# Performance work log

Measured on AMD Instinct MI355X. Metric: run time of the kernel, lower is better.

The kernel has to match this reference:

```python
import jax, jax.numpy as jnp
import numpy as np

B, N, C, H = 2, 2048, 1024, 16
D = C // H  # head_dim = 64
EPS = 1e-6


def rmsnorm(x, w, eps=EPS):
    # RMSNorm over last dim (head_dim), matching torch RMSNorm (computed in fp32)
    x32 = x.astype(jnp.float32)
    y = x32 * jax.lax.rsqrt(jnp.mean(x32 * x32, axis=-1, keepdims=True) + eps)
    return y.astype(x.dtype) * w


def setup_inputs() -> dict:
    key = jax.random.key(0)
    ks = jax.random.split(key, 4)
    return {
        "x": jax.random.normal(ks[0], (B, N, C), dtype=jnp.float32),
        "w_qkv": jax.random.normal(ks[1], (C, 3 * C), dtype=jnp.float32) * 0.02,
        "b_qkv": jnp.zeros((3 * C,), dtype=jnp.float32),
        "q_w": jnp.ones((D,), dtype=jnp.float32),
        "k_w": jnp.ones((D,), dtype=jnp.float32),
        "w_proj": jax.random.normal(ks[2], (C, C), dtype=jnp.float32) * 0.02,
        "b_proj": jnp.zeros((C,), dtype=jnp.float32),
    }


def reference(x, w_qkv, b_qkv, q_w, k_w, w_proj, b_proj):
    b, n, c = x.shape
    h, d = H, c // H
    # QKV projection -> [3, B, H, N, D]
    qkv = (x @ w_qkv + b_qkv).reshape(b, n, 3, h, d).transpose(2, 0, 3, 1, 4)
    q, k, v = qkv[0], qkv[1], qkv[2]
    # per-head RMSNorm on q/k (qk_norm=True, use_rmsnorm=True)
    q = rmsnorm(q, q_w)
    k = rmsnorm(k, k_w)
    # scaled dot-product attention (scale = head_dim**-0.5, no dropout at eval)
    scale = d ** -0.5
    attn = jax.nn.softmax(jnp.einsum('bhqd,bhkd->bhqk', q, k) * scale, axis=-1)
    out = jnp.einsum('bhqk,bhkd->bhqd', attn, v)  # [B,H,N,D]
    out = out.transpose(0, 2, 1, 3).reshape(b, n, c)
    return out @ w_proj + b_proj
```

## Files before the change

### kernel.cpp

```cpp
#include <hip/hip_runtime.h>

typedef unsigned short u16;
typedef unsigned int u32;
typedef float f4 __attribute__((ext_vector_type(4)));
typedef __bf16 b8 __attribute__((ext_vector_type(8)));
typedef _Float16 h4 __attribute__((ext_vector_type(4)));
typedef __fp16 hp2 __attribute__((ext_vector_type(2)));

#if __has_builtin(__builtin_amdgcn_exp2f)
#define EXP2(x) __builtin_amdgcn_exp2f(x)
#else
#define EXP2(x) exp2f(x)
#endif

__device__ __forceinline__ u16 f2bf(float f) {
  unsigned u = __float_as_uint(f);
  u += 0x7fffu + ((u >> 16) & 1u);
  return (u16)(u >> 16);
}
__device__ __forceinline__ float bf2f(u16 h) {
  return __uint_as_float(((unsigned)h) << 16);
}

__global__ void k_convert_all(const float* __restrict__ x,
                              const float* __restrict__ w_qkv,
                              const float* __restrict__ w_proj,
                              u16* __restrict__ xb, u16* __restrict__ wqkT,
                              u16* __restrict__ wpjT) {
  __shared__ u16 t[64][65];
  int bid = blockIdx.x;
  if (bid < 2048) {
    int i = (bid * 256 + threadIdx.x) * 8;
    float4 a = *(const float4*)(x + i);
    float4 b = *(const float4*)(x + i + 4);
    union { u16 h[8]; uint4 v; } r;
    r.h[0] = f2bf(a.x); r.h[1] = f2bf(a.y); r.h[2] = f2bf(a.z); r.h[3] = f2bf(a.w);
    r.h[4] = f2bf(b.x); r.h[5] = f2bf(b.y); r.h[6] = f2bf(b.z); r.h[7] = f2bf(b.w);
    *(uint4*)(xb + i) = r.v;
    return;
  }
  const float* w; u16* wT; int Ncols, Krows, bx, by;
  if (bid < 2816) { int l = bid - 2048; w = w_qkv; wT = wqkT; Ncols = 3072; Krows = 1024; bx = l % 48; by = l / 48; }
  else            { int l = bid - 2816; w = w_proj; wT = wpjT; Ncols = 1024; Krows = 1024; bx = l & 15; by = l >> 4; }
  int n0 = bx * 64, k0 = by * 64;
#pragma unroll
  for (int it = 0; it < 16; ++it) {
    int e = it * 256 + threadIdx.x;
    int r = e >> 6, c = e & 63;
    t[r][c] = f2bf(w[(size_t)(k0 + r) * Ncols + n0 + c]);
  }
  __syncthreads();
#pragma unroll
  for (int it = 0; it < 4; ++it) {
    int e = it * 256 + threadIdx.x;
    int r = e >> 4, c0 = (e & 15) * 4;
    union { u16 h[4]; uint2 v; } pk;
    pk.h[0] = t[c0][r]; pk.h[1] = t[c0 + 1][r];
    pk.h[2] = t[c0 + 2][r]; pk.h[3] = t[c0 + 3][r];
    *(uint2*)(wT + (size_t)(n0 + r) * Krows + k0 + c0) = pk.v;
  }
}

__global__ __launch_bounds__(256, 3) void k_gemm_qkv(
    const u16* __restrict__ A, const u16* __restrict__ Bt,
    const float* __restrict__ bias,
    u16* __restrict__ oq, u16* __restrict__ ok, u16* __restrict__ ov,
    const float* __restrict__ qw, const float* __restrict__ kw,
    int K) {
  __shared__ u16 lA[2][128 * 32];
  __shared__ u16 lB[2][128 * 32];
  const int tid = threadIdx.x;
  const int lane = tid & 63, lrow = lane & 15, lq = lane >> 4;
  const int wave = tid >> 6;
  const int bm = blockIdx.y * 128, bn = blockIdx.x * 128;
  const int wm = (wave >> 1) * 64, wn = (wave & 1) * 64;

  const int ch0 = tid, ch1 = 256 + tid;
  const u16* ap0 = A + (size_t)(bm + (ch0 >> 2)) * K + (ch0 & 3) * 8;
  const u16* ap1 = A + (size_t)(bm + (ch1 >> 2)) * K + (ch1 & 3) * 8;
  const u16* bp0 = Bt + (size_t)(bn + (ch0 >> 2)) * K + (ch0 & 3) * 8;
  const u16* bp1 = Bt + (size_t)(bn + (ch1 >> 2)) * K + (ch1 & 3) * 8;

  uint4 pA0 = *(const uint4*)ap0, pA1 = *(const uint4*)ap1;
  uint4 pB0 = *(const uint4*)bp0, pB1 = *(const uint4*)bp1;

  f4 acc[4][4] = {};
  const int iters = K >> 5;
  for (int it = 0; it < iters; ++it) {
    const int s = it & 1;
    *(uint4*)(lA[s] + ch0 * 8) = pA0; *(uint4*)(lA[s] + ch1 * 8) = pA1;
    *(uint4*)(lB[s] + ch0 * 8) = pB0; *(uint4*)(lB[s] + ch1 * 8) = pB1;
    if (it + 1 < iters) {
      ap0 += 32; ap1 += 32; bp0 += 32; bp1 += 32;
      pA0 = *(const uint4*)ap0; pA1 = *(const uint4*)ap1;
      pB0 = *(const uint4*)bp0; pB1 = *(const uint4*)bp1;
    }
    __syncthreads();
    b8 af[4], bf[4];
#pragma unroll
    for (int i = 0; i < 4; ++i)
      af[i] = *(const b8*)(lA[s] + (wm + i * 16 + lrow) * 32 + lq * 8);
#pragma unroll
    for (int j = 0; j < 4; ++j)
      bf[j] = *(const b8*)(lB[s] + (wn + j * 16 + lrow) * 32 + lq * 8);
#pragma unroll
    for (int i = 0; i < 4; ++i)
#pragma unroll
      for (int j = 0; j < 4; ++j)
        acc[i][j] = __builtin_amdgcn_mfma_f32_16x16x32_bf16(af[i], bf[j], acc[i][j], 0, 0, 0);
  }

  float bv[4];
#pragma unroll
  for (int j = 0; j < 4; ++j) bv[j] = bias[bn + wn + j * 16 + lrow];

  const float CS = 0.125f * 1.44269504088896340736f;
  const int n0w = bn + wn;
  const int sec = n0w >> 10;
  const int h = (n0w >> 6) & 15;
#pragma unroll
  for (int i = 0; i < 4; ++i) {
    float v[4][4];
#pragma unroll
    for (int j = 0; j < 4; ++j)
#pragma unroll
      for (int r = 0; r < 4; ++r) v[j][r] = acc[i][j][r] + bv[j];
    if (sec < 2) {
      u16* dst = sec == 0 ? oq : ok;
      const float* w = sec == 0 ? qw : kw;
      float ex = sec == 0 ? CS : 1.0f;
#pragma unroll
      for (int r = 0; r < 4; ++r) {
        float ss = v[0][r] * v[0][r] + v[1][r] * v[1][r] +
                   v[2][r] * v[2][r] + v[3][r] * v[3][r];
        ss += __shfl_xor(ss, 1, 64); ss += __shfl_xor(ss, 2, 64);
        ss += __shfl_xor(ss, 4, 64); ss += __shfl_xor(ss, 8, 64);
        float sc = rsqrtf(ss * (1.0f / 64.0f) + 1e-6f) * ex;
        int m = bm + wm + i * 16 + lq * 4 + r;
        int bb = m >> 11, ns = m & 2047;
        u16* rowp = dst + ((size_t)(bb * 16 + h) * 2048 + ns) * 64;
#pragma unroll
        for (int j = 0; j < 4; ++j) {
          int d = j * 16 + lrow;
          rowp[d] = f2bf(v[j][r] * sc * w[d]);
        }
      }
    } else {
      int m0 = bm + wm + i * 16 + lq * 4;
      int bb = m0 >> 11, ns = m0 & 2047;
#pragma unroll
      for (int j = 0; j < 4; ++j) {
        int d = j * 16 + lrow;
        union { _Float16 hh[4]; uint2 u; } pk;
#pragma unroll
        for (int r = 0; r < 4; ++r) pk.hh[r] = (_Float16)v[j][r];
        *(uint2*)(ov + ((size_t)(bb * 16 + h) * 64 + d) * 2048 + ns) = pk.u;
      }
    }
  }
}

__global__ __launch_bounds__(256, 4) void k_gemm2(
    const u16* __restrict__ A, const u16* __restrict__ Bt,
    const float* __restrict__ bias, float* __restrict__ outF,
    int K, int Ncols) {
  __shared__ u16 lA[2][64 * 32];
  __shared__ u16 lB[2][128 * 32];
  const int tid = threadIdx.x;
  const int lane = tid & 63, lrow = lane & 15, lq = lane >> 4;
  const int wave = tid >> 6;
  const int bm = blockIdx.y * 64, bn = blockIdx.x * 128;
  const int wm = (wave >> 1) * 32, wn = (wave & 1) * 64;

  const int cha = tid;
  const int ch0 = tid, ch1 = 256 + tid;
  const u16* ap = A + (size_t)(bm + (cha >> 2)) * K + (cha & 3) * 8;
  const u16* bp0 = Bt + (size_t)(bn + (ch0 >> 2)) * K + (ch0 & 3) * 8;
  const u16* bp1 = Bt + (size_t)(bn + (ch1 >> 2)) * K + (ch1 & 3) * 8;

  uint4 pA = *(const uint4*)ap;
  uint4 pB0 = *(const uint4*)bp0, pB1 = *(const uint4*)bp1;

  f4 acc[2][4] = {};
  const int iters = K >> 5;
  for (int it = 0; it < iters; ++it) {
    const int s = it & 1;
    *(uint4*)(lA[s] + cha * 8) = pA;
    *(uint4*)(lB[s] + ch0 * 8) = pB0; *(uint4*)(lB[s] + ch1 * 8) = pB1;
    if (it + 1 < iters) {
      ap += 32; bp0 += 32; bp1 += 32;
      pA = *(const uint4*)ap;
      pB0 = *(const uint4*)bp0; pB1 = *(const uint4*)bp1;
    }
    __syncthreads();
    b8 af[2], bf[4];
#pragma unroll
    for (int i = 0; i < 2; ++i)
      af[i] = *(const b8*)(lA[s] + (wm + i * 16 + lrow) * 32 + lq * 8);
#pragma unroll
    for (int j = 0; j < 4; ++j)
      bf[j] = *(const b8*)(lB[s] + (wn + j * 16 + lrow) * 32 + lq * 8);
#pragma unroll
    for (int i = 0; i < 2; ++i)
#pragma unroll
      for (int j = 0; j < 4; ++j)
        acc[i][j] = __builtin_amdgcn_mfma_f32_16x16x32_bf16(af[i], bf[j], acc[i][j], 0, 0, 0);
  }
#pragma unroll
  for (int i = 0; i < 2; ++i)
#pragma unroll
    for (int j = 0; j < 4; ++j) {
      int n = bn + wn + j * 16 + lrow;
      float bv = bias[n];
#pragma unroll
      for (int r = 0; r < 4; ++r) {
        int m = bm + wm + i * 16 + lq * 4 + r;
        outF[(size_t)m * Ncols + n] = acc[i][j][r] + bv;
      }
    }
}

__global__ __launch_bounds__(512, 8) void k_attn(
    const u16* __restrict__ qb, const u16* __restrict__ kb,
    const u16* __restrict__ vt, u16* __restrict__ ao) {
  __shared__ u16 lK[128 * 72];
  __shared__ u16 lV[64 * 140];
  const int bh = blockIdx.y;
  const int q0 = blockIdx.x * 64;
  const int tid = threadIdx.x, wave = tid >> 6, lane = tid & 63;
  const int lrow = lane & 15, lq = lane >> 4;
  const int qg = wave & 3;
  const int kh = wave >> 2;
  const int wq = qg * 16;

  b8 qf[2];
#pragma unroll
  for (int ks = 0; ks < 2; ++ks)
    qf[ks] = *(const b8*)(qb + ((size_t)bh * 2048 + q0 + wq + lrow) * 64 + ks * 32 + lq * 8);

  f4 o[4] = {};
  f4 lacc = {};
  h4 ones;
  ones[0] = (_Float16)1.0f; ones[1] = (_Float16)1.0f;
  ones[2] = (_Float16)1.0f; ones[3] = (_Float16)1.0f;

  const int ch0 = tid, ch1 = 512 + tid;
  const u16* kp0 = kb + (size_t)bh * 2048 * 64 + (size_t)(ch0 >> 3) * 64 + (ch0 & 7) * 8;
  const u16* kp1 = kb + (size_t)bh * 2048 * 64 + (size_t)(ch1 >> 3) * 64 + (ch1 & 7) * 8;
  const u16* vp0 = vt + (size_t)bh * 64 * 2048 + (size_t)(ch0 >> 4) * 2048 + (ch0 & 15) * 8;
  const u16* vp1 = vt + (size_t)bh * 64 * 2048 + (size_t)(ch1 >> 4) * 2048 + (ch1 & 15) * 8;
  u16* lKw0 = lK + (ch0 >> 3) * 72 + (ch0 & 7) * 8;
  u16* lKw1 = lK + (ch1 >> 3) * 72 + (ch1 & 7) * 8;
  u16* lVw0 = lV + (ch0 >> 4) * 140 + (ch0 & 15) * 8;
  u16* lVw1 = lV + (ch1 >> 4) * 140 + (ch1 & 15) * 8;

  uint4 pK0 = *(const uint4*)kp0, pK1 = *(const uint4*)kp1;
  uint4 pV0 = *(const uint4*)vp0, pV1 = *(const uint4*)vp1;

  for (int it = 0; it < 16; ++it) {
    *(uint4*)lKw0 = pK0;
    *(uint4*)lKw1 = pK1;
    *(uint2*)lVw0 = make_uint2(pV0.x, pV0.y);
    *(uint2*)(lVw0 + 4) = make_uint2(pV0.z, pV0.w);
    *(uint2*)lVw1 = make_uint2(pV1.x, pV1.y);
    *(uint2*)(lVw1 + 4) = make_uint2(pV1.z, pV1.w);
    __syncthreads();

    if (it < 15) {
      kp0 += 128 * 64; kp1 += 128 * 64; vp0 += 128; vp1 += 128;
      pK0 = *(const uint4*)kp0; pK1 = *(const uint4*)kp1;
      pV0 = *(const uint4*)vp0; pV1 = *(const uint4*)vp1;
    }

    f4 st[4] = {};
#pragma unroll
    for (int ks = 0; ks < 2; ++ks)
#pragma unroll
      for (int kt = 0; kt < 4; ++kt) {
        b8 kf = *(const b8*)(lK + ((kh * 64 + kt * 16) + lrow) * 72 + ks * 32 + lq * 8);
        st[kt] = __builtin_amdgcn_mfma_f32_16x16x32_bf16(kf, qf[ks], st[kt], 0, 0, 0);
      }
#pragma unroll
    for (int kt = 0; kt < 4; ++kt) {
      union { hp2 p2[2]; h4 v; } cv;
      cv.p2[0] = __builtin_amdgcn_cvt_pkrtz(EXP2(st[kt][0]), EXP2(st[kt][1]));
      cv.p2[1] = __builtin_amdgcn_cvt_pkrtz(EXP2(st[kt][2]), EXP2(st[kt][3]));
      h4 pf = cv.v;
      lacc = __builtin_amdgcn_mfma_f32_16x16x16f16(ones, pf, lacc, 0, 0, 0);
#pragma unroll
      for (int dt = 0; dt < 4; ++dt) {
        h4 va = *(const h4*)(lV + (dt * 16 + lrow) * 140 + kh * 64 + kt * 16 + lq * 4);
        o[dt] = __builtin_amdgcn_mfma_f32_16x16x16f16(va, pf, o[dt], 0, 0, 0);
      }
    }
    __syncthreads();
  }

  float* ms = (float*)lK;
  const int base = (qg * 64 + lane) * 17;
  if (kh) {
#pragma unroll
    for (int dt = 0; dt < 4; ++dt)
#pragma unroll
      for (int rr = 0; rr < 4; ++rr) ms[base + dt * 4 + rr] = o[dt][rr];
    ms[base + 16] = lacc[0];
  }
  __syncthreads();
  if (!kh) {
    float inv = 1.0f / (lacc[0] + ms[base + 16]);
    const int bb = bh >> 4, h = bh & 15;
    int q = q0 + wq + lrow;
#pragma unroll
    for (int dt = 0; dt < 4; ++dt) {
      union { u16 h2[4]; uint2 v; } r;
#pragma unroll
      for (int rr = 0; rr < 4; ++rr)
        r.h2[rr] = f2bf((o[dt][rr] + ms[base + dt * 4 + rr]) * inv);
      *(uint2*)(ao + ((size_t)bb * 2048 + q) * 1024 + h * 64 + dt * 16 + lq * 4) = r.v;
    }
  }
}

extern "C" void kernel_launch(void* const* d_in, const int* in_sizes, int n_in,
                              void* d_out, int out_size, void* d_ws, size_t ws_size,
                              hipStream_t stream) {
  const float* x      = (const float*)d_in[0];
  const float* w_qkv  = (const float*)d_in[1];
  const float* b_qkv  = (const float*)d_in[2];
  const float* q_w    = (const float*)d_in[3];
  const float* k_w    = (const float*)d_in[4];
  const float* w_proj = (const float*)d_in[5];
  const float* b_proj = (const float*)d_in[6];
  float* out = (float*)d_out;

  u16* xb   = (u16*)d_ws;
  u16* wqkT = xb + 4194304;
  u16* wpjT = wqkT + 3145728;
  u16* qb   = wpjT + 1048576;
  u16* kb   = qb + 4194304;
  u16* vtb  = kb + 4194304;
  u16* ao   = xb;

  k_convert_all<<<3072, 256, 0, stream>>>(x, w_qkv, w_proj, xb, wqkT, wpjT);
  k_gemm_qkv<<<dim3(24, 32), 256, 0, stream>>>(xb, wqkT, b_qkv, qb, kb, vtb, q_w, k_w, 1024);
  k_attn<<<dim3(32, 32), 512, 0, stream>>>(qb, kb, vtb, ao);
  k_gemm2<<<dim3(8, 64), 256, 0, stream>>>(ao, wpjT, b_proj, out, 1024, 1024);
}
```

Baseline: 195.3 us.

## Enlarge attention query tile to 256 rows and drop key-split reduction

Each attention block now processes 256 queries instead of 64, with each wave owning 32 query rows over the full 128-key tile rather than splitting keys across two wave halves. This reuses each K/V tile loaded into LDS across four times as many queries and removes the cross-wave LDS merge of partial outputs and sums at the end. In exchange the grid drops to 256 blocks, about one per CU on this device, and register pressure roughly doubles per wave, which may reduce occupancy and latency hiding.

```diff
diff --git a/kernel.cpp b/kernel.cpp
--- a/kernel.cpp
+++ b/kernel.cpp
@@ -220,26 +220,27 @@
     }
 }
 
-__global__ __launch_bounds__(512, 8) void k_attn(
+__global__ __launch_bounds__(512, 2) void k_attn(
     const u16* __restrict__ qb, const u16* __restrict__ kb,
     const u16* __restrict__ vt, u16* __restrict__ ao) {
   __shared__ u16 lK[128 * 72];
   __shared__ u16 lV[64 * 140];
   const int bh = blockIdx.y;
-  const int q0 = blockIdx.x * 64;
+  const int q0 = blockIdx.x * 256;
   const int tid = threadIdx.x, wave = tid >> 6, lane = tid & 63;
   const int lrow = lane & 15, lq = lane >> 4;
-  const int qg = wave & 3;
-  const int kh = wave >> 2;
-  const int wq = qg * 16;
-
-  b8 qf[2];
-#pragma unroll
-  for (int ks = 0; ks < 2; ++ks)
-    qf[ks] = *(const b8*)(qb + ((size_t)bh * 2048 + q0 + wq + lrow) * 64 + ks * 32 + lq * 8);
-
-  f4 o[4] = {};
-  f4 lacc = {};
+  const int wq = wave * 32;
+
+  b8 qf[2][2];
+#pragma unroll
+  for (int g = 0; g < 2; ++g)
+#pragma unroll
+    for (int ks = 0; ks < 2; ++ks)
+      qf[g][ks] = *(const b8*)(qb + ((size_t)bh * 2048 + q0 + wq + g * 16 + lrow) * 64 +
+                               ks * 32 + lq * 8);
+
+  f4 o[2][4] = {};
+  f4 lacc[2] = {};
   h4 ones;
   ones[0] = (_Float16)1.0f; ones[1] = (_Float16)1.0f;
   ones[2] = (_Float16)1.0f; ones[3] = (_Float16)1.0f;
@@ -272,50 +273,51 @@
       pV0 = *(const uint4*)vp0; pV1 = *(const uint4*)vp1;
     }
 
-    f4 st[4] = {};
+    f4 st[2][8] = {};
 #pragma unroll
     for (int ks = 0; ks < 2; ++ks)
 #pragma unroll
-      for (int kt = 0; kt < 4; ++kt) {
-        b8 kf = *(const b8*)(lK + ((kh * 64 + kt * 16) + lrow) * 72 + ks * 32 + lq * 8);
-        st[kt] = __builtin_amdgcn_mfma_f32_16x16x32_bf16(kf, qf[ks], st[kt], 0, 0, 0);
-      }
-#pragma unroll
-    for (int kt = 0; kt < 4; ++kt) {
-      union { hp2 p2[2]; h4 v; } cv;
-      cv.p2[0] = __builtin_amdgcn_cvt_pkrtz(EXP2(st[kt][0]), EXP2(st[kt][1]));
-      cv.p2[1] = __builtin_amdgcn_cvt_pkrtz(EXP2(st[kt][2]), EXP2(st[kt][3]));
-      h4 pf = cv.v;
-      lacc = __builtin_amdgcn_mfma_f32_16x16x16f16(ones, pf, lacc, 0, 0, 0);
+      for (int kt = 0; kt < 8; ++kt) {
+        b8 kf = *(const b8*)(lK + (kt * 16 + lrow) * 72 + ks * 32 + lq * 8);
+        st[0][kt] = __builtin_amdgcn_mfma_f32_16x16x32_bf16(kf, qf[0][ks], st[0][kt], 0, 0, 0);
+        st[1][kt] = __builtin_amdgcn_mfma_f32_16x16x32_bf16(kf, qf[1][ks], st[1][kt], 0, 0, 0);
+      }
+
+    h4 pf[2][8];
+#pragma unroll
+    for (int g = 0; g < 2; ++g)
+#pragma unroll
+      for (int kt = 0; kt < 8; ++kt) {
+        union { hp2 p2[2]; h4 v; } cv;
+        cv.p2[0] = __builtin_amdgcn_cvt_pkrtz(EXP2(st[g][kt][0]), EXP2(st[g][kt][1]));
+        cv.p2[1] = __builtin_amdgcn_cvt_pkrtz(EXP2(st[g][kt][2]), EXP2(st[g][kt][3]));
+        pf[g][kt] = cv.v;
+      }
+
+#pragma unroll
+    for (int kt = 0; kt < 8; ++kt) {
+      lacc[0] = __builtin_amdgcn_mfma_f32_16x16x16f16(ones, pf[0][kt], lacc[0], 0, 0, 0);
+      lacc[1] = __builtin_amdgcn_mfma_f32_16x16x16f16(ones, pf[1][kt], lacc[1], 0, 0, 0);
 #pragma unroll
       for (int dt = 0; dt < 4; ++dt) {
-        h4 va = *(const h4*)(lV + (dt * 16 + lrow) * 140 + kh * 64 + kt * 16 + lq * 4);
-        o[dt] = __builtin_amdgcn_mfma_f32_16x16x16f16(va, pf, o[dt], 0, 0, 0);
+        h4 va = *(const h4*)(lV + (dt * 16 + lrow) * 140 + kt * 16 + lq * 4);
+        o[0][dt] = __builtin_amdgcn_mfma_f32_16x16x16f16(va, pf[0][kt], o[0][dt], 0, 0, 0);
+        o[1][dt] = __builtin_amdgcn_mfma_f32_16x16x16f16(va, pf[1][kt], o[1][dt], 0, 0, 0);
       }
     }
     __syncthreads();
   }
 
-  float* ms = (float*)lK;
-  const int base = (qg * 64 + lane) * 17;
-  if (kh) {
-#pragma unroll
-    for (int dt = 0; dt < 4; ++dt)
-#pragma unroll
-      for (int rr = 0; rr < 4; ++rr) ms[base + dt * 4 + rr] = o[dt][rr];
-    ms[base + 16] = lacc[0];
-  }
-  __syncthreads();
-  if (!kh) {
-    float inv = 1.0f / (lacc[0] + ms[base + 16]);
-    const int bb = bh >> 4, h = bh & 15;
-    int q = q0 + wq + lrow;
+  const int bb = bh >> 4, h = bh & 15;
+#pragma unroll
+  for (int g = 0; g < 2; ++g) {
+    float inv = 1.0f / lacc[g][0];
+    int q = q0 + wq + g * 16 + lrow;
 #pragma unroll
     for (int dt = 0; dt < 4; ++dt) {
       union { u16 h2[4]; uint2 v; } r;
 #pragma unroll
-      for (int rr = 0; rr < 4; ++rr)
-        r.h2[rr] = f2bf((o[dt][rr] + ms[base + dt * 4 + rr]) * inv);
+      for (int rr = 0; rr < 4; ++rr) r.h2[rr] = f2bf(o[g][dt][rr] * inv);
       *(uint2*)(ao + ((size_t)bb * 2048 + q) * 1024 + h * 64 + dt * 16 + lq * 4) = r.v;
     }
   }
@@ -343,6 +345,6 @@
 
   k_convert_all<<<3072, 256, 0, stream>>>(x, w_qkv, w_proj, xb, wqkT, wpjT);
   k_gemm_qkv<<<dim3(24, 32), 256, 0, stream>>>(xb, wqkT, b_qkv, qb, kb, vtb, q_w, k_w, 1024);
-  k_attn<<<dim3(32, 32), 512, 0, stream>>>(qb, kb, vtb, ao);
+  k_attn<<<dim3(8, 32), 512, 0, stream>>>(qb, kb, vtb, ao);
   k_gemm2<<<dim3(8, 64), 256, 0, stream>>>(ao, wpjT, b_proj, out, 1024, 1024);
 }
```

Measured after the change: 189.7 us, median of 2. -2.8%, faster.
